# Optimization experiments

Measured on AMD Instinct MI355X. Metric: run time of the kernel, lower is better.

Reference implementation:

```python
import jax, jax.numpy as jnp
import numpy as np


def _relative_position_index(ws: int) -> jnp.ndarray:
    # (2, ws*ws) grid coords, Swin-style relative position index, shape (N, N)
    coords = jnp.stack(jnp.meshgrid(jnp.arange(ws), jnp.arange(ws), indexing='ij'))
    cf = coords.reshape(2, -1)  # (2, N)
    rel = cf[:, :, None] - cf[:, None, :]  # (2, N, N)
    return (rel[0] + ws - 1) * (2 * ws - 1) + (rel[1] + ws - 1)  # (N, N) int


def setup_inputs() -> dict:
    key = jax.random.key(0)
    ks = jax.random.split(key, 5)
    B, N, C, H, WS = 4096, 64, 128, 4, 8
    x = jax.random.normal(ks[0], (B, N, C), dtype=jnp.float32)
    qkv_w = jax.random.normal(ks[1], (C, 3 * C), dtype=jnp.float32) * (1.0 / np.sqrt(C))
    qkv_b = jnp.zeros((3 * C,), dtype=jnp.float32)
    proj_w = jax.random.normal(ks[2], (C, C), dtype=jnp.float32) * (1.0 / np.sqrt(C))
    proj_b = jnp.zeros((C,), dtype=jnp.float32)
    bias_table = jax.random.normal(ks[3], ((2 * WS - 1) ** 2, H), dtype=jnp.float32) * 0.02
    return {"x": x, "qkv_w": qkv_w, "qkv_b": qkv_b, "proj_w": proj_w,
            "proj_b": proj_b, "bias_table": bias_table,
            "window_size": WS, "num_heads": H}


def reference(x, qkv_w, qkv_b, proj_w, proj_b, bias_table, window_size, num_heads):
    B, N, C = x.shape
    H = num_heads
    D = C // H
    scale = D ** -0.5
    # QKV projection: (B, N, 3C) -> (3, B, H, N, D)
    qkv = (jnp.einsum('bnc,cf->bnf', x, qkv_w) + qkv_b)
    qkv = qkv.reshape(B, N, 3, H, D).transpose(2, 0, 3, 1, 4)
    q, k, v = qkv[0], qkv[1], qkv[2]
    # scaled QK^T: (B, H, N, N)
    attn = jnp.einsum('bhqd,bhkd->bhqk', q * scale, k)
    # relative position bias: (N, N, H) -> (1, H, N, N)
    rel_idx = _relative_position_index(window_size)
    bias = bias_table[rel_idx].transpose(2, 0, 1)[None]
    attn = jax.nn.softmax(attn + bias, axis=-1)
    # weighted sum of values: (B, H, N, D) -> (B, N, C)
    out = jnp.einsum('bhqk,bhkd->bhqd', attn, v).transpose(0, 2, 1, 3).reshape(B, N, C)
    out = jnp.einsum('bnc,cf->bnf', out, proj_w) + proj_b
    return out
```

## Files before the change

### kernel.cpp

```cpp
#include <hip/hip_runtime.h>
#include <stdint.h>


typedef __attribute__((ext_vector_type(4))) float  f32x4;
typedef __attribute__((ext_vector_type(8))) __bf16 bf16x8;

#define DEV static __device__ __forceinline__

DEV unsigned short f2bf(float f) {
  unsigned int u = __float_as_uint(f);
  u += 0x7FFFu + ((u >> 16) & 1u);
  return (unsigned short)(u >> 16);
}

DEV int xaddr (int r, int cb) { return r*256 + (cb ^ ((r & 7) << 4)); }
DEV int qkaddr(int r, int cb) { return r*64  + (cb ^ (((r >> 1) & 3) << 4)); }
DEV int vtaddr(int d, int cb) { return d*128 + (cb ^ ((d & 7) << 4)); }
DEV int paddr (int r, int cb) { return r*128 + (cb ^ ((r & 7) << 4)); }
DEV int staddr(int r, int cb) { return r*512 + (cb ^ ((r & 15) << 4)); }

template <int CTRL>
DEV float dppf(float v) {
  return __int_as_float(__builtin_amdgcn_mov_dpp(__float_as_int(v), CTRL, 0xF, 0xF, false));
}
DEV float rmax16(float v) {
  v = fmaxf(v, dppf<0x128>(v)); v = fmaxf(v, dppf<0x124>(v));
  v = fmaxf(v, dppf<0x122>(v)); v = fmaxf(v, dppf<0x121>(v));
  return v;
}
DEV float rsum16(float v) {
  v += dppf<0x128>(v); v += dppf<0x124>(v); v += dppf<0x122>(v); v += dppf<0x121>(v);
  return v;
}

DEV f32x4 mfma16(bf16x8 a, bf16x8 b, f32x4 c) {
  return __builtin_amdgcn_mfma_f32_16x16x32_bf16(a, b, c, 0, 0, 0);
}

__global__ void prep_kernel(const float* __restrict__ qkv_w, const float* __restrict__ proj_w,
                            const float* __restrict__ bias_table,
                            unsigned short* __restrict__ wq, unsigned short* __restrict__ wp,
                            float* __restrict__ bias_full) {
  int idx = blockIdx.x * 256 + threadIdx.x;
  if (idx < 49152) {
    int i = idx & 7, lane = (idx >> 3) & 63, ks = (idx >> 9) & 3, nt = idx >> 11;
    int k = ks*32 + (lane >> 4)*8 + i;
    int col = nt*16 + (lane & 15);
    wq[idx] = f2bf(qkv_w[k*384 + col]);
  } else if (idx < 65536) {
    int t = idx - 49152;
    int i = t & 7, lane = (t >> 3) & 63, ks = (t >> 9) & 3, nt = t >> 11;
    int k = ks*32 + (lane >> 4)*8 + i;
    int col = nt*16 + (lane & 15);
    wp[t] = f2bf(proj_w[k*128 + col]);
  } else if (idx < 81920) {
    int t = idx - 65536;
    int h = t >> 12, q = (t >> 6) & 63, kk = t & 63;
    int ri = q >> 3, ci = q & 7, rj = kk >> 3, cj = kk & 7;
    bias_full[t] = bias_table[((ri - rj + 7)*15 + (ci - cj + 7))*4 + h];
  }
}

__global__ __launch_bounds__(256, 2) void fused_kernel(
    const float* __restrict__ x, const float* __restrict__ qkv_b, const float* __restrict__ proj_b,
    const unsigned short* __restrict__ wq, const unsigned short* __restrict__ wp,
    const float* __restrict__ bias_full, float* __restrict__ out)
{
  __shared__ __align__(16) char lds[65536];
  const int b    = blockIdx.x;
  const int tid  = threadIdx.x;
  const int lane = tid & 63;
  const int w    = tid >> 6;
  const int l15  = lane & 15;
  const int lq   = lane >> 4;
  const float SCALE = 0.17677669529663687f;
  const f32x4 FZ = {0.f, 0.f, 0.f, 0.f};

  {
    const float4* x4 = (const float4*)(x + (size_t)b * 8192);
    #pragma unroll
    for (int it = 0; it < 8; ++it) {
      int f4 = it*256 + tid;
      int r = f4 >> 5, c4 = f4 & 31;
      float4 v = x4[f4];
      unsigned int lo = (unsigned int)f2bf(v.x) | ((unsigned int)f2bf(v.y) << 16);
      unsigned int hi = (unsigned int)f2bf(v.z) | ((unsigned int)f2bf(v.w) << 16);
      *(uint2*)(lds + xaddr(r, c4*8)) = make_uint2(lo, hi);
    }
  }
  __syncthreads();

  f32x4 acc[6][4];
  #pragma unroll
  for (int t = 0; t < 6; ++t)
    #pragma unroll
    for (int m = 0; m < 4; ++m) acc[t][m] = FZ;

  #pragma unroll
  for (int ks = 0; ks < 4; ++ks) {
    bf16x8 afr[4];
    #pragma unroll
    for (int m = 0; m < 4; ++m)
      afr[m] = *(const bf16x8*)(lds + xaddr(m*16 + l15, ks*64 + lq*16));
    #pragma unroll
    for (int t = 0; t < 6; ++t) {
      int nt = (t >> 1)*8 + 2*w + (t & 1);
      bf16x8 bfr = *(const bf16x8*)((const char*)wq + (nt*4 + ks)*1024 + lane*16);
      #pragma unroll
      for (int m = 0; m < 4; ++m)
        acc[t][m] = mfma16(afr[m], bfr, acc[t][m]);
    }
  }
  __syncthreads();

  char* qb = lds + 16384 + w*8192;
  char* kb = qb + 4096;
  char* vb = lds + 49152 + w*4096;
  #pragma unroll
  for (int t = 0; t < 2; ++t) {
    float bq = qkv_b[       (2*w + t)*16 + l15];
    float bk = qkv_b[128 + (2*w + t)*16 + l15];
    float bv = qkv_b[256 + (2*w + t)*16 + l15];
    #pragma unroll
    for (int m = 0; m < 4; ++m) {
      #pragma unroll
      for (int j = 0; j < 4; ++j) {
        int r = m*16 + lq*4 + j;
        *(unsigned short*)(qb + qkaddr(r, (t*16 + l15)*2)) = f2bf((acc[t  ][m][j] + bq) * SCALE);
        *(unsigned short*)(kb + qkaddr(r, (t*16 + l15)*2)) = f2bf( acc[t+2][m][j] + bk);
      }
      int d  = t*16 + l15;
      int r0 = m*16 + lq*4;
      unsigned int lo = (unsigned int)f2bf(acc[t+4][m][0] + bv) | ((unsigned int)f2bf(acc[t+4][m][1] + bv) << 16);
      unsigned int hi = (unsigned int)f2bf(acc[t+4][m][2] + bv) | ((unsigned int)f2bf(acc[t+4][m][3] + bv) << 16);
      *(uint2*)(vb + vtaddr(d, r0*2)) = make_uint2(lo, hi);
    }
  }

  bf16x8 aq[4], bk8[4];
  #pragma unroll
  for (int m = 0; m < 4; ++m) {
    aq [m] = *(const bf16x8*)(qb + qkaddr(m*16 + l15, lq*16));
    bk8[m] = *(const bf16x8*)(kb + qkaddr(m*16 + l15, lq*16));
  }
  f32x4 s[4][4];
  #pragma unroll
  for (int m = 0; m < 4; ++m)
    #pragma unroll
    for (int n = 0; n < 4; ++n)
      s[m][n] = mfma16(aq[m], bk8[n], FZ);

  const float* bh = bias_full + w*4096;
  #pragma unroll
  for (int m = 0; m < 4; ++m)
    #pragma unroll
    for (int j = 0; j < 4; ++j) {
      int q = m*16 + lq*4 + j;
      #pragma unroll
      for (int n = 0; n < 4; ++n)
        s[m][n][j] += bh[q*64 + n*16 + l15];
    }

  float inv[4][4];
  #pragma unroll
  for (int m = 0; m < 4; ++m)
    #pragma unroll
    for (int j = 0; j < 4; ++j) {
      float mx = fmaxf(fmaxf(s[m][0][j], s[m][1][j]), fmaxf(s[m][2][j], s[m][3][j]));
      mx = rmax16(mx);
      float sum = 0.f;
      #pragma unroll
      for (int n = 0; n < 4; ++n) {
        float p = __expf(s[m][n][j] - mx);
        s[m][n][j] = p;
        sum += p;
      }
      sum = rsum16(sum);
      inv[m][j] = __fdividef(1.f, sum);
    }

  char* pb = qb;
  #pragma unroll
  for (int m = 0; m < 4; ++m)
    #pragma unroll
    for (int n = 0; n < 4; ++n)
      #pragma unroll
      for (int j = 0; j < 4; ++j) {
        int q = m*16 + lq*4 + j;
        *(unsigned short*)(pb + paddr(q, (n*16 + l15)*2)) = f2bf(s[m][n][j]);
      }

  f32x4 o[4][2];
  #pragma unroll
  for (int m = 0; m < 4; ++m) { o[m][0] = FZ; o[m][1] = FZ; }
  #pragma unroll
  for (int ks = 0; ks < 2; ++ks) {
    bf16x8 ap[4], bv8[2];
    #pragma unroll
    for (int m = 0; m < 4; ++m)
      ap[m] = *(const bf16x8*)(pb + paddr(m*16 + l15, ks*64 + lq*16));
    #pragma unroll
    for (int n2 = 0; n2 < 2; ++n2)
      bv8[n2] = *(const bf16x8*)(vb + vtaddr(n2*16 + l15, ks*64 + lq*16));
    #pragma unroll
    for (int m = 0; m < 4; ++m)
      #pragma unroll
      for (int n2 = 0; n2 < 2; ++n2)
        o[m][n2] = mfma16(ap[m], bv8[n2], o[m][n2]);
  }

  #pragma unroll
  for (int m = 0; m < 4; ++m)
    #pragma unroll
    for (int n2 = 0; n2 < 2; ++n2)
      #pragma unroll
      for (int j = 0; j < 4; ++j) {
        int r = m*16 + lq*4 + j;
        int c = w*32 + n2*16 + l15;
        *(unsigned short*)(lds + xaddr(r, c*2)) = f2bf(o[m][n2][j] * inv[m][j]);
      }
  __syncthreads();

  f32x4 pacc[4][2];
  #pragma unroll
  for (int m = 0; m < 4; ++m) { pacc[m][0] = FZ; pacc[m][1] = FZ; }
  #pragma unroll
  for (int ks = 0; ks < 4; ++ks) {
    bf16x8 ao[4];
    #pragma unroll
    for (int m = 0; m < 4; ++m)
      ao[m] = *(const bf16x8*)(lds + xaddr(m*16 + l15, ks*64 + lq*16));
    #pragma unroll
    for (int t = 0; t < 2; ++t) {
      int nt = 2*w + t;
      bf16x8 bfr = *(const bf16x8*)((const char*)wp + (nt*4 + ks)*1024 + lane*16);
      #pragma unroll
      for (int m = 0; m < 4; ++m)
        pacc[m][t] = mfma16(ao[m], bfr, pacc[m][t]);
    }
  }

  float pb0 = proj_b[(2*w    )*16 + l15];
  float pb1 = proj_b[(2*w + 1)*16 + l15];
  #pragma unroll
  for (int m = 0; m < 4; ++m)
    #pragma unroll
    for (int t = 0; t < 2; ++t)
      #pragma unroll
      for (int j = 0; j < 4; ++j) {
        int r = m*16 + lq*4 + j;
        int c = (2*w + t)*16 + l15;
        *(float*)(lds + 16384 + staddr(r, c*4)) = pacc[m][t][j] + (t ? pb1 : pb0);
      }
  __syncthreads();

  float4* out4 = (float4*)(out + (size_t)b * 8192);
  #pragma unroll
  for (int it = 0; it < 8; ++it) {
    int f4 = it*256 + tid;
    int r = f4 >> 5, c4 = f4 & 31;
    out4[f4] = *(const float4*)(lds + 16384 + staddr(r, c4*16));
  }
}

extern "C" void kernel_launch(void* const* d_in, const int* in_sizes, int n_in,
                              void* d_out, int out_size, void* d_ws, size_t ws_size,
                              hipStream_t stream) {
  const float* x        = (const float*)d_in[0];
  const float* qkv_w    = (const float*)d_in[1];
  const float* qkv_b    = (const float*)d_in[2];
  const float* proj_w   = (const float*)d_in[3];
  const float* proj_b   = (const float*)d_in[4];
  const float* bias_tab = (const float*)d_in[5];
  float* out = (float*)d_out;

  unsigned short* wq = (unsigned short*)d_ws;
  unsigned short* wp = (unsigned short*)((char*)d_ws + 98304);
  float* bias_full   = (float*)((char*)d_ws + 131072);

  int B = in_sizes[0] / 8192;

  prep_kernel<<<320, 256, 0, stream>>>(qkv_w, proj_w, bias_tab, wq, wp, bias_full);
  fused_kernel<<<B, 256, 0, stream>>>(x, qkv_b, proj_b, wq, wp, bias_full, out);
}
```

Measured before the change: 114.0 us.

## Use transposed MFMA outputs for packed stores, cut LDS to 48KB for 3 blocks/CU

Swaps the MFMA operands for the Q, K, score, PV and projection products so each lane holds four consecutive columns. Q/K, probabilities and the attention output can then be written to LDS as packed bf16 pairs, and the final output goes straight to global memory as float4 without LDS staging. The softmax row reduction now uses two cross-lane shuffles instead of DPP trees, and the probabilities reuse the Q/K buffer. LDS drops from 64KB to 48KB with launch bounds raised to 3 blocks per CU to improve occupancy, at the risk of register spills and less coalesced output stores.

```diff
diff --git a/kernel.cpp b/kernel.cpp
--- a/kernel.cpp
+++ b/kernel.cpp
@@ -13,25 +13,16 @@
   return (unsigned short)(u >> 16);
 }
 
+DEV unsigned int pk2(float a, float b) {
+  __bf16 x = (__bf16)a, y = (__bf16)b;
+  unsigned short ux = __builtin_bit_cast(unsigned short, x);
+  unsigned short uy = __builtin_bit_cast(unsigned short, y);
+  return (unsigned int)ux | ((unsigned int)uy << 16);
+}
+
 DEV int xaddr (int r, int cb) { return r*256 + (cb ^ ((r & 7) << 4)); }
-DEV int qkaddr(int r, int cb) { return r*64  + (cb ^ (((r >> 1) & 3) << 4)); }
+DEV int qkaddr(int r, int cb) { return r*128 + (cb ^ ((r & 7) << 4)); }
 DEV int vtaddr(int d, int cb) { return d*128 + (cb ^ ((d & 7) << 4)); }
-DEV int paddr (int r, int cb) { return r*128 + (cb ^ ((r & 7) << 4)); }
-DEV int staddr(int r, int cb) { return r*512 + (cb ^ ((r & 15) << 4)); }
-
-template <int CTRL>
-DEV float dppf(float v) {
-  return __int_as_float(__builtin_amdgcn_mov_dpp(__float_as_int(v), CTRL, 0xF, 0xF, false));
-}
-DEV float rmax16(float v) {
-  v = fmaxf(v, dppf<0x128>(v)); v = fmaxf(v, dppf<0x124>(v));
-  v = fmaxf(v, dppf<0x122>(v)); v = fmaxf(v, dppf<0x121>(v));
-  return v;
-}
-DEV float rsum16(float v) {
-  v += dppf<0x128>(v); v += dppf<0x124>(v); v += dppf<0x122>(v); v += dppf<0x121>(v);
-  return v;
-}
 
 DEV f32x4 mfma16(bf16x8 a, bf16x8 b, f32x4 c) {
   return __builtin_amdgcn_mfma_f32_16x16x32_bf16(a, b, c, 0, 0, 0);
@@ -61,12 +52,12 @@
   }
 }
 
-__global__ __launch_bounds__(256, 2) void fused_kernel(
+__global__ __launch_bounds__(256, 3) void fused_kernel(
     const float* __restrict__ x, const float* __restrict__ qkv_b, const float* __restrict__ proj_b,
     const unsigned short* __restrict__ wq, const unsigned short* __restrict__ wp,
     const float* __restrict__ bias_full, float* __restrict__ out)
 {
-  __shared__ __align__(16) char lds[65536];
+  __shared__ __align__(16) char lds[49152];
   const int b    = blockIdx.x;
   const int tid  = threadIdx.x;
   const int lane = tid & 63;
@@ -83,183 +74,195 @@
       int f4 = it*256 + tid;
       int r = f4 >> 5, c4 = f4 & 31;
       float4 v = x4[f4];
-      unsigned int lo = (unsigned int)f2bf(v.x) | ((unsigned int)f2bf(v.y) << 16);
-      unsigned int hi = (unsigned int)f2bf(v.z) | ((unsigned int)f2bf(v.w) << 16);
-      *(uint2*)(lds + xaddr(r, c4*8)) = make_uint2(lo, hi);
-    }
-  }
-  __syncthreads();
-
-  f32x4 acc[6][4];
-  #pragma unroll
-  for (int t = 0; t < 6; ++t)
-    #pragma unroll
-    for (int m = 0; m < 4; ++m) acc[t][m] = FZ;
+      *(uint2*)(lds + xaddr(r, c4*8)) = make_uint2(pk2(v.x, v.y), pk2(v.z, v.w));
+    }
+  }
+  __syncthreads();
+
+  f32x4 qacc[2][4], kacc[2][4], vacc[4][2];
+  #pragma unroll
+  for (int t = 0; t < 2; ++t)
+    #pragma unroll
+    for (int m = 0; m < 4; ++m) { qacc[t][m] = FZ; kacc[t][m] = FZ; }
+  #pragma unroll
+  for (int m = 0; m < 4; ++m) { vacc[m][0] = FZ; vacc[m][1] = FZ; }
 
   #pragma unroll
   for (int ks = 0; ks < 4; ++ks) {
-    bf16x8 afr[4];
-    #pragma unroll
-    for (int m = 0; m < 4; ++m)
-      afr[m] = *(const bf16x8*)(lds + xaddr(m*16 + l15, ks*64 + lq*16));
-    #pragma unroll
-    for (int t = 0; t < 6; ++t) {
-      int nt = (t >> 1)*8 + 2*w + (t & 1);
-      bf16x8 bfr = *(const bf16x8*)((const char*)wq + (nt*4 + ks)*1024 + lane*16);
-      #pragma unroll
-      for (int m = 0; m < 4; ++m)
-        acc[t][m] = mfma16(afr[m], bfr, acc[t][m]);
-    }
-  }
-  __syncthreads();
-
-  char* qb = lds + 16384 + w*8192;
-  char* kb = qb + 4096;
-  char* vb = lds + 49152 + w*4096;
+    bf16x8 xfr[4];
+    #pragma unroll
+    for (int m = 0; m < 4; ++m)
+      xfr[m] = *(const bf16x8*)(lds + xaddr(m*16 + l15, ks*64 + lq*16));
+    #pragma unroll
+    for (int t = 0; t < 2; ++t) {
+      bf16x8 wfq = *(const bf16x8*)((const char*)wq + (((2*w + t)*4      + ks)*64 + lane)*16);
+      bf16x8 wfk = *(const bf16x8*)((const char*)wq + (((8 + 2*w + t)*4  + ks)*64 + lane)*16);
+      bf16x8 wfv = *(const bf16x8*)((const char*)wq + (((16 + 2*w + t)*4 + ks)*64 + lane)*16);
+      #pragma unroll
+      for (int m = 0; m < 4; ++m) {
+        qacc[t][m] = mfma16(wfq, xfr[m], qacc[t][m]);
+        kacc[t][m] = mfma16(wfk, xfr[m], kacc[t][m]);
+        vacc[m][t] = mfma16(xfr[m], wfv, vacc[m][t]);
+      }
+    }
+  }
+  __syncthreads();
+
+  char* qkb = lds + 16384 + w*8192;
+  char* vtb = lds + w*4096;
   #pragma unroll
   for (int t = 0; t < 2; ++t) {
-    float bq = qkv_b[       (2*w + t)*16 + l15];
-    float bk = qkv_b[128 + (2*w + t)*16 + l15];
-    float bv = qkv_b[256 + (2*w + t)*16 + l15];
-    #pragma unroll
-    for (int m = 0; m < 4; ++m) {
+    float4 bq4 = *(const float4*)(qkv_b +        w*32 + t*16 + lq*4);
+    float4 bk4 = *(const float4*)(qkv_b + 128 +  w*32 + t*16 + lq*4);
+    #pragma unroll
+    for (int m = 0; m < 4; ++m) {
+      int row = m*16 + l15;
+      int cb  = (t*16 + lq*4)*2;
+      *(unsigned int*)(qkb + qkaddr(row, cb))
+          = pk2((qacc[t][m][0] + bq4.x)*SCALE, (qacc[t][m][1] + bq4.y)*SCALE);
+      *(unsigned int*)(qkb + qkaddr(row, cb + 4))
+          = pk2((qacc[t][m][2] + bq4.z)*SCALE, (qacc[t][m][3] + bq4.w)*SCALE);
+      *(unsigned int*)(qkb + qkaddr(row, 64 + cb))
+          = pk2(kacc[t][m][0] + bk4.x, kacc[t][m][1] + bk4.y);
+      *(unsigned int*)(qkb + qkaddr(row, 64 + cb + 4))
+          = pk2(kacc[t][m][2] + bk4.z, kacc[t][m][3] + bk4.w);
+    }
+  }
+  #pragma unroll
+  for (int dt = 0; dt < 2; ++dt) {
+    float bv = qkv_b[256 + w*32 + dt*16 + l15];
+    #pragma unroll
+    for (int m = 0; m < 4; ++m) {
+      *(uint2*)(vtb + vtaddr(dt*16 + l15, (m*16 + lq*4)*2)) =
+        make_uint2(pk2(vacc[m][dt][0] + bv, vacc[m][dt][1] + bv),
+                   pk2(vacc[m][dt][2] + bv, vacc[m][dt][3] + bv));
+    }
+  }
+
+  bf16x8 qf[4], kf[4];
+  #pragma unroll
+  for (int m = 0; m < 4; ++m) {
+    qf[m] = *(const bf16x8*)(qkb + qkaddr(m*16 + l15,      lq*16));
+    kf[m] = *(const bf16x8*)(qkb + qkaddr(m*16 + l15, 64 + lq*16));
+  }
+  f32x4 s[4][4];
+  #pragma unroll
+  for (int n = 0; n < 4; ++n)
+    #pragma unroll
+    for (int m = 0; m < 4; ++m)
+      s[n][m] = mfma16(kf[n], qf[m], FZ);
+
+  const float* bh = bias_full + w*4096;
+  #pragma unroll
+  for (int n = 0; n < 4; ++n)
+    #pragma unroll
+    for (int m = 0; m < 4; ++m) {
+      float4 b4 = *(const float4*)(bh + (m*16 + l15)*64 + n*16 + lq*4);
+      s[n][m][0] += b4.x; s[n][m][1] += b4.y; s[n][m][2] += b4.z; s[n][m][3] += b4.w;
+    }
+
+  float inv_[4];
+  #pragma unroll
+  for (int m = 0; m < 4; ++m) {
+    float mx = s[0][m][0];
+    #pragma unroll
+    for (int n = 0; n < 4; ++n)
+      #pragma unroll
+      for (int j = 0; j < 4; ++j) mx = fmaxf(mx, s[n][m][j]);
+    mx = fmaxf(mx, __shfl_xor(mx, 16));
+    mx = fmaxf(mx, __shfl_xor(mx, 32));
+    float sum = 0.f;
+    #pragma unroll
+    for (int n = 0; n < 4; ++n)
       #pragma unroll
       for (int j = 0; j < 4; ++j) {
-        int r = m*16 + lq*4 + j;
-        *(unsigned short*)(qb + qkaddr(r, (t*16 + l15)*2)) = f2bf((acc[t  ][m][j] + bq) * SCALE);
-        *(unsigned short*)(kb + qkaddr(r, (t*16 + l15)*2)) = f2bf( acc[t+2][m][j] + bk);
-      }
-      int d  = t*16 + l15;
-      int r0 = m*16 + lq*4;
-      unsigned int lo = (unsigned int)f2bf(acc[t+4][m][0] + bv) | ((unsigned int)f2bf(acc[t+4][m][1] + bv) << 16);
-      unsigned int hi = (unsigned int)f2bf(acc[t+4][m][2] + bv) | ((unsigned int)f2bf(acc[t+4][m][3] + bv) << 16);
-      *(uint2*)(vb + vtaddr(d, r0*2)) = make_uint2(lo, hi);
-    }
-  }
-
-  bf16x8 aq[4], bk8[4];
-  #pragma unroll
-  for (int m = 0; m < 4; ++m) {
-    aq [m] = *(const bf16x8*)(qb + qkaddr(m*16 + l15, lq*16));
-    bk8[m] = *(const bf16x8*)(kb + qkaddr(m*16 + l15, lq*16));
-  }
-  f32x4 s[4][4];
-  #pragma unroll
-  for (int m = 0; m < 4; ++m)
-    #pragma unroll
-    for (int n = 0; n < 4; ++n)
-      s[m][n] = mfma16(aq[m], bk8[n], FZ);
-
-  const float* bh = bias_full + w*4096;
-  #pragma unroll
-  for (int m = 0; m < 4; ++m)
-    #pragma unroll
-    for (int j = 0; j < 4; ++j) {
-      int q = m*16 + lq*4 + j;
-      #pragma unroll
-      for (int n = 0; n < 4; ++n)
-        s[m][n][j] += bh[q*64 + n*16 + l15];
-    }
-
-  float inv[4][4];
-  #pragma unroll
-  for (int m = 0; m < 4; ++m)
-    #pragma unroll
-    for (int j = 0; j < 4; ++j) {
-      float mx = fmaxf(fmaxf(s[m][0][j], s[m][1][j]), fmaxf(s[m][2][j], s[m][3][j]));
-      mx = rmax16(mx);
-      float sum = 0.f;
-      #pragma unroll
-      for (int n = 0; n < 4; ++n) {
-        float p = __expf(s[m][n][j] - mx);
-        s[m][n][j] = p;
+        float p = __expf(s[n][m][j] - mx);
+        s[n][m][j] = p;
         sum += p;
       }
-      sum = rsum16(sum);
-      inv[m][j] = __fdividef(1.f, sum);
-    }
-
-  char* pb = qb;
-  #pragma unroll
-  for (int m = 0; m < 4; ++m)
-    #pragma unroll
-    for (int n = 0; n < 4; ++n)
-      #pragma unroll
-      for (int j = 0; j < 4; ++j) {
-        int q = m*16 + lq*4 + j;
-        *(unsigned short*)(pb + paddr(q, (n*16 + l15)*2)) = f2bf(s[m][n][j]);
-      }
-
-  f32x4 o[4][2];
-  #pragma unroll
-  for (int m = 0; m < 4; ++m) { o[m][0] = FZ; o[m][1] = FZ; }
+    sum += __shfl_xor(sum, 16);
+    sum += __shfl_xor(sum, 32);
+    inv_[m] = __fdividef(1.f, sum);
+  }
+
+  #pragma unroll
+  for (int n = 0; n < 4; ++n)
+    #pragma unroll
+    for (int m = 0; m < 4; ++m) {
+      int row = m*16 + l15;
+      int cb  = (n*16 + lq*4)*2;
+      *(unsigned int*)(qkb + qkaddr(row, cb))     = pk2(s[n][m][0], s[n][m][1]);
+      *(unsigned int*)(qkb + qkaddr(row, cb + 4)) = pk2(s[n][m][2], s[n][m][3]);
+    }
+
+  f32x4 o[2][4];
+  #pragma unroll
+  for (int dt = 0; dt < 2; ++dt)
+    #pragma unroll
+    for (int m = 0; m < 4; ++m) o[dt][m] = FZ;
   #pragma unroll
   for (int ks = 0; ks < 2; ++ks) {
-    bf16x8 ap[4], bv8[2];
-    #pragma unroll
-    for (int m = 0; m < 4; ++m)
-      ap[m] = *(const bf16x8*)(pb + paddr(m*16 + l15, ks*64 + lq*16));
-    #pragma unroll
-    for (int n2 = 0; n2 < 2; ++n2)
-      bv8[n2] = *(const bf16x8*)(vb + vtaddr(n2*16 + l15, ks*64 + lq*16));
-    #pragma unroll
-    for (int m = 0; m < 4; ++m)
-      #pragma unroll
-      for (int n2 = 0; n2 < 2; ++n2)
-        o[m][n2] = mfma16(ap[m], bv8[n2], o[m][n2]);
-  }
-
-  #pragma unroll
-  for (int m = 0; m < 4; ++m)
-    #pragma unroll
-    for (int n2 = 0; n2 < 2; ++n2)
-      #pragma unroll
-      for (int j = 0; j < 4; ++j) {
-        int r = m*16 + lq*4 + j;
-        int c = w*32 + n2*16 + l15;
-        *(unsigned short*)(lds + xaddr(r, c*2)) = f2bf(o[m][n2][j] * inv[m][j]);
-      }
-  __syncthreads();
-
-  f32x4 pacc[4][2];
-  #pragma unroll
-  for (int m = 0; m < 4; ++m) { pacc[m][0] = FZ; pacc[m][1] = FZ; }
+    bf16x8 vf[2], pf[4];
+    #pragma unroll
+    for (int dt = 0; dt < 2; ++dt)
+      vf[dt] = *(const bf16x8*)(vtb + vtaddr(dt*16 + l15, ks*64 + lq*16));
+    #pragma unroll
+    for (int m = 0; m < 4; ++m)
+      pf[m] = *(const bf16x8*)(qkb + qkaddr(m*16 + l15, ks*64 + lq*16));
+    #pragma unroll
+    for (int dt = 0; dt < 2; ++dt)
+      #pragma unroll
+      for (int m = 0; m < 4; ++m)
+        o[dt][m] = mfma16(vf[dt], pf[m], o[dt][m]);
+  }
+  __syncthreads();
+
+  #pragma unroll
+  for (int dt = 0; dt < 2; ++dt)
+    #pragma unroll
+    for (int m = 0; m < 4; ++m) {
+      int row = m*16 + l15;
+      int cb  = (w*32 + dt*16 + lq*4)*2;
+      *(unsigned int*)(lds + xaddr(row, cb))
+          = pk2(o[dt][m][0]*inv_[m], o[dt][m][1]*inv_[m]);
+      *(unsigned int*)(lds + xaddr(row, cb + 4))
+          = pk2(o[dt][m][2]*inv_[m], o[dt][m][3]*inv_[m]);
+    }
+  __syncthreads();
+
+  f32x4 pacc[2][4];
+  #pragma unroll
+  for (int t = 0; t < 2; ++t)
+    #pragma unroll
+    for (int m = 0; m < 4; ++m) pacc[t][m] = FZ;
   #pragma unroll
   for (int ks = 0; ks < 4; ++ks) {
-    bf16x8 ao[4];
-    #pragma unroll
-    for (int m = 0; m < 4; ++m)
-      ao[m] = *(const bf16x8*)(lds + xaddr(m*16 + l15, ks*64 + lq*16));
+    bf16x8 ofr[4];
+    #pragma unroll
+    for (int m = 0; m < 4; ++m)
+      ofr[m] = *(const bf16x8*)(lds + xaddr(m*16 + l15, ks*64 + lq*16));
     #pragma unroll
     for (int t = 0; t < 2; ++t) {
-      int nt = 2*w + t;
-      bf16x8 bfr = *(const bf16x8*)((const char*)wp + (nt*4 + ks)*1024 + lane*16);
+      bf16x8 wf = *(const bf16x8*)((const char*)wp + (((2*w + t)*4 + ks)*64 + lane)*16);
       #pragma unroll
       for (int m = 0; m < 4; ++m)
-        pacc[m][t] = mfma16(ao[m], bfr, pacc[m][t]);
-    }
-  }
-
-  float pb0 = proj_b[(2*w    )*16 + l15];
-  float pb1 = proj_b[(2*w + 1)*16 + l15];
-  #pragma unroll
-  for (int m = 0; m < 4; ++m)
-    #pragma unroll
-    for (int t = 0; t < 2; ++t)
-      #pragma unroll
-      for (int j = 0; j < 4; ++j) {
-        int r = m*16 + lq*4 + j;
-        int c = (2*w + t)*16 + l15;
-        *(float*)(lds + 16384 + staddr(r, c*4)) = pacc[m][t][j] + (t ? pb1 : pb0);
-      }
-  __syncthreads();
-
-  float4* out4 = (float4*)(out + (size_t)b * 8192);
-  #pragma unroll
-  for (int it = 0; it < 8; ++it) {
-    int f4 = it*256 + tid;
-    int r = f4 >> 5, c4 = f4 & 31;
-    out4[f4] = *(const float4*)(lds + 16384 + staddr(r, c4*16));
+        pacc[t][m] = mfma16(wf, ofr[m], pacc[t][m]);
+    }
+  }
+
+  float* ob = out + (size_t)b * 8192;
+  #pragma unroll
+  for (int t = 0; t < 2; ++t) {
+    float4 pb4 = *(const float4*)(proj_b + (2*w + t)*16 + lq*4);
+    #pragma unroll
+    for (int m = 0; m < 4; ++m) {
+      float4 v;
+      v.x = pacc[t][m][0] + pb4.x;
+      v.y = pacc[t][m][1] + pb4.y;
+      v.z = pacc[t][m][2] + pb4.z;
+      v.w = pacc[t][m][3] + pb4.w;
+      *(float4*)(ob + (m*16 + l15)*128 + (2*w + t)*16 + lq*4) = v;
+    }
   }
 }
 
```

After: 115.6 us. About the same (+1.4%).
